# Performance work log

Hardware: AMD Instinct MI355X
Metric: run time of the kernel (lower is better)

Reference implementation:

```python
import jax, jax.numpy as jnp
import numpy as np

N_NODES = 50000
N_EDGES = 800000
N_GRAPHS = 256
DIMS = [64, 128, 256, 512]
GRU_H = 256


def _linit(key, shape, fan_in):
    lim = 1.0 / np.sqrt(fan_in)
    return jax.random.uniform(key, shape, jnp.float32, -lim, lim)


def setup_inputs() -> dict:
    key = jax.random.key(0)
    ks = jax.random.split(key, 24)
    x = jax.random.normal(ks[0], (N_NODES, DIMS[0]), jnp.float32)
    edge_index = jax.random.randint(ks[1], (2, N_EDGES), 0, N_NODES, jnp.int64)
    batch_idx = jnp.sort(jax.random.randint(ks[2], (N_NODES,), 0, N_GRAPHS, jnp.int64))
    inp = {"x": x, "edge_index": edge_index, "batch_idx": batch_idx}
    # GCN layer weights (stored [in, out]) and biases
    for i in range(3):
        inp[f"gcn_w{i}"] = _linit(ks[3 + i], (DIMS[i], DIMS[i + 1]), DIMS[i])
        inp[f"gcn_b{i}"] = jnp.zeros((DIMS[i + 1],), jnp.float32)
    # gate nn: Linear(512, 1)
    inp["gate_w"] = _linit(ks[6], (DIMS[3], 1), DIMS[3])
    inp["gate_b"] = jnp.zeros((1,), jnp.float32)
    # GRU: 2 layers, torch layout W_ih [3H, in], W_hh [3H, H]
    ins = [DIMS[3], GRU_H]
    for l in range(2):
        inp[f"gru_wih{l}"] = _linit(ks[7 + 4 * l], (3 * GRU_H, ins[l]), GRU_H)
        inp[f"gru_whh{l}"] = _linit(ks[8 + 4 * l], (3 * GRU_H, GRU_H), GRU_H)
        inp[f"gru_bih{l}"] = _linit(ks[9 + 4 * l], (3 * GRU_H,), GRU_H)
        inp[f"gru_bhh{l}"] = _linit(ks[10 + 4 * l], (3 * GRU_H,), GRU_H)
    # output proj: Linear(256, 512), torch layout [out, in]
    inp["proj_w"] = _linit(ks[15], (DIMS[3], GRU_H), GRU_H)
    inp["proj_b"] = jnp.zeros((DIMS[3],), jnp.float32)
    return inp


def _gcn_norm(edge_index, n_nodes):
    # add self-loops, symmetric normalization (PyG GCNConv default)
    loop = jnp.arange(n_nodes, dtype=edge_index.dtype)
    src = jnp.concatenate([edge_index[0], loop])
    dst = jnp.concatenate([edge_index[1], loop])
    deg = jax.ops.segment_sum(jnp.ones_like(dst, jnp.float32), dst, num_segments=n_nodes)
    dinv = jnp.where(deg > 0, jax.lax.rsqrt(jnp.maximum(deg, 1.0)), 0.0)
    norm = dinv[src] * dinv[dst]
    return src, dst, norm


def _gru_cell(xv, h, wih, whh, bih, bhh):
    gi = xv @ wih.T + bih
    gh = h @ whh.T + bhh
    ir, iz, inn = jnp.split(gi, 3, axis=-1)
    hr, hz, hn = jnp.split(gh, 3, axis=-1)
    r = jax.nn.sigmoid(ir + hr)
    z = jax.nn.sigmoid(iz + hz)
    n = jnp.tanh(inn + r * hn)
    return (1.0 - z) * n + z * h


def reference(x, edge_index, batch_idx,
              gcn_w0, gcn_b0, gcn_w1, gcn_b1, gcn_w2, gcn_b2,
              gate_w, gate_b,
              gru_wih0, gru_whh0, gru_bih0, gru_bhh0,
              gru_wih1, gru_whh1, gru_bih1, gru_bhh1,
              proj_w, proj_b):
    n = x.shape[0]
    src, dst, norm = _gcn_norm(edge_index, n)
    for w, b in ((gcn_w0, gcn_b0), (gcn_w1, gcn_b1), (gcn_w2, gcn_b2)):
        h = x @ w                                  # [N, out]
        msg = h[src] * norm[:, None]               # gather over edges
        x = jax.ops.segment_sum(msg, dst, num_segments=n) + b
        x = jax.nn.relu(x)
    # attentional aggregation: segment softmax over gate scores
    gate = (x @ gate_w + gate_b)[:, 0]             # [N]
    gmax = jax.ops.segment_max(gate, batch_idx, num_segments=N_GRAPHS)
    e = jnp.exp(gate - gmax[batch_idx])
    denom = jax.ops.segment_sum(e, batch_idx, num_segments=N_GRAPHS)
    alpha = e / denom[batch_idx]
    graph_emb = jax.ops.segment_sum(x * alpha[:, None], batch_idx, num_segments=N_GRAPHS)  # [G, 512]
    # 2-layer GRU with seq_len=1, h0=0
    h0 = jnp.zeros((N_GRAPHS, GRU_H), x.dtype)
    h1 = _gru_cell(graph_emb, h0, gru_wih0, gru_whh0, gru_bih0, gru_bhh0)
    h2 = _gru_cell(h1, h0, gru_wih1, gru_whh1, gru_bih1, gru_bhh1)
    return h2 @ proj_w.T + proj_b                  # [G, 512]
```

## Files before the change

kernel.cpp:

```cpp
#include <hip/hip_runtime.h>


#define N_GRAPHS 256
#define GRU_H 256
#define SCAN_CHUNK 2048

typedef __attribute__((ext_vector_type(8))) short short8;
typedef __attribute__((ext_vector_type(4))) float floatx4;

typedef unsigned short ushort_t;
typedef unsigned int uint_t;

__device__ __forceinline__ float bflo(uint_t u) { return __uint_as_float(u << 16); }
__device__ __forceinline__ float bfhi(uint_t u) { return __uint_as_float(u & 0xffff0000u); }
__device__ __forceinline__ uint_t f2bf(float f) {
    uint_t u = __float_as_uint(f);
    return (u + 0x7fffu + ((u >> 16) & 1u)) >> 16;
}
__device__ __forceinline__ uint_t pack2(float a, float b) {
    return f2bf(a) | (f2bf(b) << 16);
}


__global__ void k_hist(const int* __restrict__ dst, int* __restrict__ counts, int E) {
    int e = blockIdx.x * blockDim.x + threadIdx.x;
    if (e < E) atomicAdd(&counts[dst[e]], 1);
}

__global__ __launch_bounds__(256) void k_scan1(const int* __restrict__ counts,
                                               int* __restrict__ rowptr,
                                               int* __restrict__ bsums,
                                               float* __restrict__ dinv, int n) {
    int b = blockIdx.x, t = threadIdx.x;
    int base = b * SCAN_CHUNK + t * 8;
    int v[8];
    int s = 0;
#pragma unroll
    for (int j = 0; j < 8; ++j) {
        int i = base + j;
        int c = (i < n) ? counts[i] : 0;
        v[j] = s;
        s += c;
        if (i < n) dinv[i] = rsqrtf((float)(c + 1));
    }
    __shared__ int sd[256];
    sd[t] = s;
    __syncthreads();
    for (int off = 1; off < 256; off <<= 1) {
        int tmp = (t >= off) ? sd[t - off] : 0;
        __syncthreads();
        sd[t] += tmp;
        __syncthreads();
    }
    int texcl = sd[t] - s;
    if (t == 255) bsums[b] = sd[255];
#pragma unroll
    for (int j = 0; j < 8; ++j) {
        int i = base + j;
        if (i < n) rowptr[i] = texcl + v[j];
    }
}

__global__ __launch_bounds__(256) void k_scan3(int* __restrict__ rowptr,
                                               int* __restrict__ cursor,
                                               const int* __restrict__ bsums,
                                               int n, int nb) {
    int b = blockIdx.x, t = threadIdx.x;
    __shared__ int s_off;
    if (t == 0) {
        int off = 0, tot = 0;
        for (int i = 0; i < nb; ++i) {
            int v = bsums[i];
            if (i < b) off += v;
            tot += v;
        }
        s_off = off;
        if (b == 0) rowptr[n] = tot;
    }
    __syncthreads();
    int off = s_off;
    int base = b * SCAN_CHUNK + t * 8;
#pragma unroll
    for (int j = 0; j < 8; ++j) {
        int i = base + j;
        if (i < n) { int r = rowptr[i] + off; rowptr[i] = r; cursor[i] = r; }
    }
}

__global__ void k_fill(const int* __restrict__ src, const int* __restrict__ dst,
                       int* __restrict__ cursor, int* __restrict__ col, int E) {
    int e = blockIdx.x * blockDim.x + threadIdx.x;
    if (e < E) {
        int pos = atomicAdd(&cursor[dst[e]], 1);
        col[pos] = src[e];
    }
}


__global__ void k_wt_all(const float* __restrict__ w0, const float* __restrict__ w1,
                         const float* __restrict__ w2, ushort_t* __restrict__ wt0,
                         ushort_t* __restrict__ wt1, ushort_t* __restrict__ wt2) {
    int idx = blockIdx.x * blockDim.x + threadIdx.x;
    if (idx < 8192) {
        int k = idx >> 7, n = idx & 127;
        wt0[(size_t)n * 64 + k] = (ushort_t)f2bf(w0[idx]);
    } else if (idx < 40960) {
        int i = idx - 8192;
        int k = i >> 8, n = i & 255;
        wt1[(size_t)n * 128 + k] = (ushort_t)f2bf(w1[i]);
    } else if (idx < 172032) {
        int i = idx - 40960;
        int k = i >> 9, n = i & 511;
        wt2[(size_t)n * 256 + k] = (ushort_t)f2bf(w2[i]);
    }
}


__global__ void k_split_all(const float* __restrict__ wih0, const float* __restrict__ wih1,
                            const float* __restrict__ pw,
                            ushort_t* __restrict__ h0, ushort_t* __restrict__ l0,
                            ushort_t* __restrict__ h1, ushort_t* __restrict__ l1,
                            ushort_t* __restrict__ h2, ushort_t* __restrict__ l2) {
    int idx = blockIdx.x * blockDim.x + threadIdx.x;
    const float* s; ushort_t* H; ushort_t* L; int i;
    if (idx < 393216)      { s = wih0; H = h0; L = l0; i = idx; }
    else if (idx < 589824) { s = wih1; H = h1; L = l1; i = idx - 393216; }
    else if (idx < 720896) { s = pw;   H = h2; L = l2; i = idx - 589824; }
    else return;
    float v = s[i];
    uint_t h = f2bf(v);
    H[i] = (ushort_t)h;
    L[i] = (ushort_t)f2bf(v - __uint_as_float(h << 16));
}


__global__ void k_prescale(const float4* __restrict__ x, const float* __restrict__ dinv,
                           uint4* __restrict__ xs, int N) {
    int idx = blockIdx.x * blockDim.x + threadIdx.x;
    int n = idx >> 3;
    if (n >= N) return;
    float dn = dinv[n];
    float4 v0 = x[idx * 2], v1 = x[idx * 2 + 1];
    uint4 o;
    o.x = pack2(v0.x * dn, v0.y * dn);
    o.y = pack2(v0.z * dn, v0.w * dn);
    o.z = pack2(v1.x * dn, v1.y * dn);
    o.w = pack2(v1.z * dn, v1.w * dn);
    xs[idx] = o;
}


__device__ __forceinline__ void acc8(float& a0, float& a1, float& a2, float& a3,
                                     float& a4, float& a5, float& a6, float& a7,
                                     const uint4& v) {
    a0 += bflo(v.x); a1 += bfhi(v.x); a2 += bflo(v.y); a3 += bfhi(v.y);
    a4 += bflo(v.z); a5 += bfhi(v.z); a6 += bflo(v.w); a7 += bfhi(v.w);
}

__global__ void k_gather_bf16(const uint4* __restrict__ xs, const int* __restrict__ rp,
                              const int* __restrict__ col, const float* __restrict__ dinv,
                              uint4* __restrict__ agg, int N, int shift ) {
    int idx = blockIdx.x * blockDim.x + threadIdx.x;
    int n = idx >> shift;
    if (n >= N) return;
    int c = idx & ((1 << shift) - 1);
    int C8 = 1 << shift;
    int a = rp[n], b = rp[n + 1];
    uint4 u = xs[(size_t)n * C8 + c];
    float a0 = bflo(u.x), a1 = bfhi(u.x), a2 = bflo(u.y), a3 = bfhi(u.y);
    float a4 = bflo(u.z), a5 = bfhi(u.z), a6 = bflo(u.w), a7 = bfhi(u.w);
    int k = a;
    for (; k + 8 <= b; k += 8) {
        int ci[8];
#pragma unroll
        for (int j = 0; j < 8; ++j) ci[j] = col[k + j];
        uint4 v[8];
#pragma unroll
        for (int j = 0; j < 8; ++j) v[j] = xs[(size_t)ci[j] * C8 + c];
#pragma unroll
        for (int j = 0; j < 8; ++j)
            acc8(a0, a1, a2, a3, a4, a5, a6, a7, v[j]);
    }
    for (; k + 4 <= b; k += 4) {
        int ci[4];
#pragma unroll
        for (int j = 0; j < 4; ++j) ci[j] = col[k + j];
        uint4 v[4];
#pragma unroll
        for (int j = 0; j < 4; ++j) v[j] = xs[(size_t)ci[j] * C8 + c];
#pragma unroll
        for (int j = 0; j < 4; ++j)
            acc8(a0, a1, a2, a3, a4, a5, a6, a7, v[j]);
    }
    for (; k < b; ++k) {
        uint4 v = xs[(size_t)col[k] * C8 + c];
        acc8(a0, a1, a2, a3, a4, a5, a6, a7, v);
    }
    float dn = dinv[n];
    uint4 o;
    o.x = pack2(a0 * dn, a1 * dn);
    o.y = pack2(a2 * dn, a3 * dn);
    o.z = pack2(a4 * dn, a5 * dn);
    o.w = pack2(a6 * dn, a7 * dn);
    agg[idx] = o;
}


__global__ __launch_bounds__(256) void k_gemm_mfma(
    const ushort_t* __restrict__ A, const ushort_t* __restrict__ Wt,
    const float* __restrict__ bias, const float* __restrict__ dinv,
    ushort_t* __restrict__ C, int M, int K, int Nout, int scale_out,
    const float* __restrict__ gate_w, float* __restrict__ gateArr) {
    __shared__ ushort_t As[64 * 72];
    __shared__ ushort_t Bs[64 * 72];
    int tid = threadIdx.x;
    int wave = tid >> 6, lane = tid & 63;
    int quad = lane >> 4, lr = lane & 15;
    int wm = (wave & 1) * 32, wn = (wave >> 1) * 32;
    int bm = blockIdx.x * 64, bn = blockIdx.y * 64;

    floatx4 zero = {0.f, 0.f, 0.f, 0.f};
    floatx4 acc00 = zero, acc01 = zero, acc10 = zero, acc11 = zero;

    int r0 = tid >> 3,         ko0 = (tid & 7) * 8;
    int r1 = (tid + 256) >> 3, ko1 = ((tid + 256) & 7) * 8;

    for (int k0 = 0; k0 < K; k0 += 64) {
        int ar0 = min(bm + r0, M - 1);
        int ar1 = min(bm + r1, M - 1);
        uint4 av0 = *(const uint4*)(A + (size_t)ar0 * K + k0 + ko0);
        uint4 av1 = *(const uint4*)(A + (size_t)ar1 * K + k0 + ko1);
        uint4 bv0 = *(const uint4*)(Wt + (size_t)(bn + r0) * K + k0 + ko0);
        uint4 bv1 = *(const uint4*)(Wt + (size_t)(bn + r1) * K + k0 + ko1);
        __syncthreads();
        *(uint4*)&As[r0 * 72 + ko0] = av0;
        *(uint4*)&As[r1 * 72 + ko1] = av1;
        *(uint4*)&Bs[r0 * 72 + ko0] = bv0;
        *(uint4*)&Bs[r1 * 72 + ko1] = bv1;
        __syncthreads();
#pragma unroll
        for (int ks = 0; ks < 2; ++ks) {
            short8 af0 = *(short8*)&As[(wm + lr) * 72 + ks * 32 + quad * 8];
            short8 af1 = *(short8*)&As[(wm + 16 + lr) * 72 + ks * 32 + quad * 8];
            short8 bf0 = *(short8*)&Bs[(wn + lr) * 72 + ks * 32 + quad * 8];
            short8 bf1 = *(short8*)&Bs[(wn + 16 + lr) * 72 + ks * 32 + quad * 8];
            acc00 = __builtin_amdgcn_mfma_f32_16x16x32_bf16(af0, bf0, acc00, 0, 0, 0);
            acc01 = __builtin_amdgcn_mfma_f32_16x16x32_bf16(af0, bf1, acc01, 0, 0, 0);
            acc10 = __builtin_amdgcn_mfma_f32_16x16x32_bf16(af1, bf0, acc10, 0, 0, 0);
            acc11 = __builtin_amdgcn_mfma_f32_16x16x32_bf16(af1, bf1, acc11, 0, 0, 0);
        }
    }

    float gwv[2] = {0.f, 0.f};
    if (gate_w) {
        gwv[0] = gate_w[bn + wn + lr];
        gwv[1] = gate_w[bn + wn + 16 + lr];
    }
    float pg[2][4] = {};
#pragma unroll
    for (int mi = 0; mi < 2; ++mi) {
#pragma unroll
        for (int ni = 0; ni < 2; ++ni) {
            floatx4 acc = (mi == 0) ? (ni == 0 ? acc00 : acc01)
                                    : (ni == 0 ? acc10 : acc11);
            int col = bn + wn + ni * 16 + lr;
            float bcol = bias[col];
#pragma unroll
            for (int r = 0; r < 4; ++r) {
                int row = bm + wm + mi * 16 + quad * 4 + r;
                if (row < M) {
                    float v = acc[r] + bcol;
                    v = fmaxf(v, 0.0f);
                    if (gate_w) pg[mi][r] += v * gwv[ni];
                    if (scale_out) v *= dinv[row];
                    C[(size_t)row * Nout + col] = (ushort_t)f2bf(v);
                }
            }
        }
    }
    if (gate_w) {
#pragma unroll
        for (int mi = 0; mi < 2; ++mi) {
#pragma unroll
            for (int r = 0; r < 4; ++r) {
                float p = pg[mi][r];
                p += __shfl_down(p, 8, 16);
                p += __shfl_down(p, 4, 16);
                p += __shfl_down(p, 2, 16);
                p += __shfl_down(p, 1, 16);
                if (lr == 0) {
                    int row = bm + wm + mi * 16 + quad * 4 + r;
                    if (row < M) atomicAdd(&gateArr[row], p);
                }
            }
        }
    }
}


__global__ __launch_bounds__(256) void k_gemm3(
    const ushort_t* __restrict__ Ahi, const ushort_t* __restrict__ Alo,
    const ushort_t* __restrict__ Whi, const ushort_t* __restrict__ Wlo,
    const float* __restrict__ bias, float* __restrict__ C,
    int M, int K, int Nout) {
    __shared__ ushort_t AsH[64 * 72];
    __shared__ ushort_t AsL[64 * 72];
    __shared__ ushort_t BsH[64 * 72];
    __shared__ ushort_t BsL[64 * 72];
    int tid = threadIdx.x;
    int wave = tid >> 6, lane = tid & 63;
    int quad = lane >> 4, lr = lane & 15;
    int wm = (wave & 1) * 32, wn = (wave >> 1) * 32;
    int bm = blockIdx.x * 64, bn = blockIdx.y * 64;

    floatx4 zero = {0.f, 0.f, 0.f, 0.f};
    floatx4 acc00 = zero, acc01 = zero, acc10 = zero, acc11 = zero;

    int r0 = tid >> 3,         ko0 = (tid & 7) * 8;
    int r1 = (tid + 256) >> 3, ko1 = ((tid + 256) & 7) * 8;

    for (int k0 = 0; k0 < K; k0 += 64) {
        int ar0 = min(bm + r0, M - 1);
        int ar1 = min(bm + r1, M - 1);
        size_t a0o = (size_t)ar0 * K + k0 + ko0, a1o = (size_t)ar1 * K + k0 + ko1;
        size_t b0o = (size_t)(bn + r0) * K + k0 + ko0, b1o = (size_t)(bn + r1) * K + k0 + ko1;
        uint4 ah0 = *(const uint4*)(Ahi + a0o), ah1 = *(const uint4*)(Ahi + a1o);
        uint4 al0 = *(const uint4*)(Alo + a0o), al1 = *(const uint4*)(Alo + a1o);
        uint4 bh0 = *(const uint4*)(Whi + b0o), bh1 = *(const uint4*)(Whi + b1o);
        uint4 bl0 = *(const uint4*)(Wlo + b0o), bl1 = *(const uint4*)(Wlo + b1o);
        __syncthreads();
        *(uint4*)&AsH[r0 * 72 + ko0] = ah0; *(uint4*)&AsH[r1 * 72 + ko1] = ah1;
        *(uint4*)&AsL[r0 * 72 + ko0] = al0; *(uint4*)&AsL[r1 * 72 + ko1] = al1;
        *(uint4*)&BsH[r0 * 72 + ko0] = bh0; *(uint4*)&BsH[r1 * 72 + ko1] = bh1;
        *(uint4*)&BsL[r0 * 72 + ko0] = bl0; *(uint4*)&BsL[r1 * 72 + ko1] = bl1;
        __syncthreads();
#pragma unroll
        for (int ks = 0; ks < 2; ++ks) {
            int a0i = (wm + lr) * 72 + ks * 32 + quad * 8;
            int a1i = (wm + 16 + lr) * 72 + ks * 32 + quad * 8;
            int b0i = (wn + lr) * 72 + ks * 32 + quad * 8;
            int b1i = (wn + 16 + lr) * 72 + ks * 32 + quad * 8;
            short8 afh0 = *(short8*)&AsH[a0i], afh1 = *(short8*)&AsH[a1i];
            short8 afl0 = *(short8*)&AsL[a0i], afl1 = *(short8*)&AsL[a1i];
            short8 bfh0 = *(short8*)&BsH[b0i], bfh1 = *(short8*)&BsH[b1i];
            short8 bfl0 = *(short8*)&BsL[b0i], bfl1 = *(short8*)&BsL[b1i];
            acc00 = __builtin_amdgcn_mfma_f32_16x16x32_bf16(afh0, bfh0, acc00, 0, 0, 0);
            acc00 = __builtin_amdgcn_mfma_f32_16x16x32_bf16(afh0, bfl0, acc00, 0, 0, 0);
            acc00 = __builtin_amdgcn_mfma_f32_16x16x32_bf16(afl0, bfh0, acc00, 0, 0, 0);
            acc01 = __builtin_amdgcn_mfma_f32_16x16x32_bf16(afh0, bfh1, acc01, 0, 0, 0);
            acc01 = __builtin_amdgcn_mfma_f32_16x16x32_bf16(afh0, bfl1, acc01, 0, 0, 0);
            acc01 = __builtin_amdgcn_mfma_f32_16x16x32_bf16(afl0, bfh1, acc01, 0, 0, 0);
            acc10 = __builtin_amdgcn_mfma_f32_16x16x32_bf16(afh1, bfh0, acc10, 0, 0, 0);
            acc10 = __builtin_amdgcn_mfma_f32_16x16x32_bf16(afh1, bfl0, acc10, 0, 0, 0);
            acc10 = __builtin_amdgcn_mfma_f32_16x16x32_bf16(afl1, bfh0, acc10, 0, 0, 0);
            acc11 = __builtin_amdgcn_mfma_f32_16x16x32_bf16(afh1, bfh1, acc11, 0, 0, 0);
            acc11 = __builtin_amdgcn_mfma_f32_16x16x32_bf16(afh1, bfl1, acc11, 0, 0, 0);
            acc11 = __builtin_amdgcn_mfma_f32_16x16x32_bf16(afl1, bfh1, acc11, 0, 0, 0);
        }
    }

#pragma unroll
    for (int mi = 0; mi < 2; ++mi) {
#pragma unroll
        for (int ni = 0; ni < 2; ++ni) {
            floatx4 acc = (mi == 0) ? (ni == 0 ? acc00 : acc01)
                                    : (ni == 0 ? acc10 : acc11);
            int col = bn + wn + ni * 16 + lr;
            float bcol = bias ? bias[col] : 0.0f;
#pragma unroll
            for (int r = 0; r < 4; ++r) {
                int row = bm + wm + mi * 16 + quad * 4 + r;
                if (row < M)
                    C[(size_t)row * Nout + col] = acc[r] + bcol;
            }
        }
    }
}


__global__ void k_gru_ep(const float* __restrict__ gi, const float* __restrict__ bih,
                         const float* __restrict__ bhh,
                         ushort_t* __restrict__ hhi, ushort_t* __restrict__ hlo, int G) {
    int idx = blockIdx.x * blockDim.x + threadIdx.x;
    int g = idx >> 8, j = idx & 255;
    if (g >= G) return;
    const float* row = gi + (size_t)g * 768;
    float ir = row[j]       + bih[j]       + bhh[j];
    float iz = row[j + 256] + bih[j + 256] + bhh[j + 256];
    float in = row[j + 512] + bih[j + 512];
    float r = 1.0f / (1.0f + expf(-ir));
    float z = 1.0f / (1.0f + expf(-iz));
    float nn = tanhf(in + r * bhh[j + 512]);
    float h = (1.0f - z) * nn;
    uint_t hi = f2bf(h);
    hhi[idx] = (ushort_t)hi;
    hlo[idx] = (ushort_t)f2bf(h - __uint_as_float(hi << 16));
}


__global__ __launch_bounds__(256) void k_softmax_emb(
    const uint_t* __restrict__ x , const float* __restrict__ gate,
    const int* __restrict__ batch, int N,
    ushort_t* __restrict__ embH, ushort_t* __restrict__ embL) {
    int g = blockIdx.x;
    int s, e;
    {
        int lo = 0, hi = N;
        while (lo < hi) { int mid = (lo + hi) >> 1; if (batch[mid] < g) lo = mid + 1; else hi = mid; }
        s = lo;
        lo = s; hi = N;
        while (lo < hi) { int mid = (lo + hi) >> 1; if (batch[mid] < g + 1) lo = mid + 1; else hi = mid; }
        e = lo;
    }
    __shared__ float red[256];
    __shared__ float sal[256];
    int tid = threadIdx.x;
    float m = -INFINITY;
    for (int i = s + tid; i < e; i += 256) m = fmaxf(m, gate[i]);
    red[tid] = m; __syncthreads();
    for (int off = 128; off > 0; off >>= 1) {
        if (tid < off) red[tid] = fmaxf(red[tid], red[tid + off]);
        __syncthreads();
    }
    m = red[0]; __syncthreads();
    float ssum = 0.f;
    for (int i = s + tid; i < e; i += 256) ssum += expf(gate[i] - m);
    red[tid] = ssum; __syncthreads();
    for (int off = 128; off > 0; off >>= 1) {
        if (tid < off) red[tid] += red[tid + off];
        __syncthreads();
    }
    float denom = red[0];
    float inv = (denom > 0.f) ? 1.0f / denom : 0.0f;
    float acc0 = 0.f, acc1 = 0.f;
    for (int base = s; base < e; base += 256) {
        int i = base + tid;
        __syncthreads();
        sal[tid] = (i < e) ? expf(gate[i] - m) * inv : 0.0f;
        __syncthreads();
        int cnt = min(256, e - base);
        for (int k = 0; k < cnt; ++k) {
            float a = sal[k];
            uint_t u = x[(size_t)(base + k) * 256 + tid];
            acc0 += a * bflo(u);
            acc1 += a * bfhi(u);
        }
    }
    int i0 = g * 512 + tid * 2;
    uint_t h0 = f2bf(acc0);
    uint_t h1 = f2bf(acc1);
    embH[i0]     = (ushort_t)h0;
    embH[i0 + 1] = (ushort_t)h1;
    embL[i0]     = (ushort_t)f2bf(acc0 - __uint_as_float(h0 << 16));
    embL[i0 + 1] = (ushort_t)f2bf(acc1 - __uint_as_float(h1 << 16));
}


extern "C" void kernel_launch(void* const* d_in, const int* in_sizes, int n_in,
                              void* d_out, int out_size, void* d_ws, size_t ws_size,
                              hipStream_t stream) {
    const float* x       = (const float*)d_in[0];
    const int*   ei      = (const int*)d_in[1];
    const int*   batch   = (const int*)d_in[2];
    const float* w0      = (const float*)d_in[3];
    const float* b0      = (const float*)d_in[4];
    const float* w1      = (const float*)d_in[5];
    const float* b1      = (const float*)d_in[6];
    const float* w2      = (const float*)d_in[7];
    const float* b2      = (const float*)d_in[8];
    const float* gate_w  = (const float*)d_in[9];
    const float* wih0    = (const float*)d_in[11];
    const float* bih0    = (const float*)d_in[13];
    const float* bhh0    = (const float*)d_in[14];
    const float* wih1    = (const float*)d_in[15];
    const float* bih1    = (const float*)d_in[17];
    const float* bhh1    = (const float*)d_in[18];
    const float* pw      = (const float*)d_in[19];
    const float* pb      = (const float*)d_in[20];
    float* out = (float*)d_out;

    const int N = in_sizes[2];
    const int E = in_sizes[1] / 2;
    const int G = N_GRAPHS;

    char* base = (char*)d_ws;
    size_t off = 0;
    auto alloc = [&](size_t bytes) -> char* {
        char* p = base + off;
        off = (off + bytes + 255) & ~(size_t)255;
        return p;
    };
    ushort_t* bufA  = (ushort_t*)alloc((size_t)N * 512 * 2);
    ushort_t* bufB  = (ushort_t*)alloc((size_t)N * 512 * 2);
    float* dinv     = (float*)alloc((size_t)N * 4);
    float* gateArr  = (float*)alloc((size_t)N * 4);
    int*   counts   = (int*)alloc((size_t)(N + 1) * 4);
    int*   cursor   = (int*)alloc((size_t)(N + 1) * 4);
    int*   rowptr   = (int*)alloc((size_t)(N + 1) * 4);
    int*   bsums    = (int*)alloc((size_t)256 * 4);
    int*   col      = (int*)alloc((size_t)E * 4);
    ushort_t* wt0   = (ushort_t*)alloc((size_t)128 * 64 * 2);
    ushort_t* wt1   = (ushort_t*)alloc((size_t)256 * 128 * 2);
    ushort_t* wt2   = (ushort_t*)alloc((size_t)512 * 256 * 2);
    ushort_t* ih0H  = (ushort_t*)alloc((size_t)768 * 512 * 2);
    ushort_t* ih0L  = (ushort_t*)alloc((size_t)768 * 512 * 2);
    ushort_t* ih1H  = (ushort_t*)alloc((size_t)768 * 256 * 2);
    ushort_t* ih1L  = (ushort_t*)alloc((size_t)768 * 256 * 2);
    ushort_t* pwH   = (ushort_t*)alloc((size_t)512 * 256 * 2);
    ushort_t* pwL   = (ushort_t*)alloc((size_t)512 * 256 * 2);
    ushort_t* embH  = (ushort_t*)alloc((size_t)G * 512 * 2);
    ushort_t* embL  = (ushort_t*)alloc((size_t)G * 512 * 2);
    ushort_t* h1H   = (ushort_t*)alloc((size_t)G * 256 * 2);
    ushort_t* h1L   = (ushort_t*)alloc((size_t)G * 256 * 2);
    ushort_t* h2H   = (ushort_t*)alloc((size_t)G * 256 * 2);
    ushort_t* h2L   = (ushort_t*)alloc((size_t)G * 256 * 2);
    float* gi       = (float*)alloc((size_t)G * 768 * 4);
    (void)ws_size; (void)n_in; (void)out_size;

    const int* src = ei;
    const int* dst = ei + E;

    const int nb = (N + SCAN_CHUNK - 1) / SCAN_CHUNK;

    size_t zbytes = (size_t)((char*)counts - (char*)gateArr) + (size_t)(N + 1) * 4;
    hipMemsetAsync(gateArr, 0, zbytes, stream);

    k_hist<<<(E + 255) / 256, 256, 0, stream>>>(dst, counts, E);
    k_scan1<<<nb, 256, 0, stream>>>(counts, rowptr, bsums, dinv, N);
    k_scan3<<<nb, 256, 0, stream>>>(rowptr, cursor, bsums, N, nb);
    k_fill<<<(E + 255) / 256, 256, 0, stream>>>(src, dst, cursor, col, E);
    k_wt_all<<<(172032 + 255) / 256, 256, 0, stream>>>(w0, w1, w2, wt0, wt1, wt2);
    k_split_all<<<(720896 + 255) / 256, 256, 0, stream>>>(wih0, wih1, pw,
                                                          ih0H, ih0L, ih1H, ih1L, pwH, pwL);

    int mBlocks = (N + 63) / 64;

    k_prescale<<<(N * 8 + 255) / 256, 256, 0, stream>>>((const float4*)x, dinv, (uint4*)bufA, N);
    k_gather_bf16<<<(N * 8 + 255) / 256, 256, 0, stream>>>((const uint4*)bufA, rowptr, col, dinv, (uint4*)bufB, N, 3);
    k_gemm_mfma<<<dim3(mBlocks, 2), 256, 0, stream>>>(bufB, wt0, b0, dinv, bufA, N, 64, 128, 1, nullptr, nullptr);

    k_gather_bf16<<<(N * 16 + 255) / 256, 256, 0, stream>>>((const uint4*)bufA, rowptr, col, dinv, (uint4*)bufB, N, 4);
    k_gemm_mfma<<<dim3(mBlocks, 4), 256, 0, stream>>>(bufB, wt1, b1, dinv, bufA, N, 128, 256, 1, nullptr, nullptr);

    k_gather_bf16<<<(N * 32 + 255) / 256, 256, 0, stream>>>((const uint4*)bufA, rowptr, col, dinv, (uint4*)bufB, N, 5);
    k_gemm_mfma<<<dim3(mBlocks, 8), 256, 0, stream>>>(bufB, wt2, b2, dinv, bufA, N, 256, 512, 0, gate_w, gateArr);

    k_softmax_emb<<<G, 256, 0, stream>>>((const uint_t*)bufA, gateArr, batch, N, embH, embL);

    k_gemm3<<<dim3(G / 64, 12), 256, 0, stream>>>(embH, embL, ih0H, ih0L, nullptr, gi, G, 512, 768);
    k_gru_ep<<<G, 256, 0, stream>>>(gi, bih0, bhh0, h1H, h1L, G);

    k_gemm3<<<dim3(G / 64, 12), 256, 0, stream>>>(h1H, h1L, ih1H, ih1L, nullptr, gi, G, 256, 768);
    k_gru_ep<<<G, 256, 0, stream>>>(gi, bih1, bhh1, h2H, h2L, G);

    k_gemm3<<<dim3(G / 64, 8), 256, 0, stream>>>(h2H, h2L, pwH, pwL, pb, out, G, 256, 512);
}
```

Baseline: 446.8 us.

## Fuse preprocessing kernels and merge tail into persistent kernel with grid barriers

Combines edge fill, input prescale, weight transpose and weight split into a single launch partitioned by block index. Replaces the softmax-embedding, three small GEMMs and two GRU epilogues with one persistent 256-block kernel synchronized by atomic spin grid barriers. This removes several kernel launches and inter-kernel gaps, at the cost of relying on all blocks being co-resident and paying barrier spin overhead.

```diff
diff --git a/kernel.cpp b/kernel.cpp
--- a/kernel.cpp
+++ b/kernel.cpp
@@ -87,66 +87,67 @@
     }
 }
 
-__global__ void k_fill(const int* __restrict__ src, const int* __restrict__ dst,
-                       int* __restrict__ cursor, int* __restrict__ col, int E) {
-    int e = blockIdx.x * blockDim.x + threadIdx.x;
-    if (e < E) {
-        int pos = atomicAdd(&cursor[dst[e]], 1);
-        col[pos] = src[e];
-    }
-}
-
-
-__global__ void k_wt_all(const float* __restrict__ w0, const float* __restrict__ w1,
-                         const float* __restrict__ w2, ushort_t* __restrict__ wt0,
-                         ushort_t* __restrict__ wt1, ushort_t* __restrict__ wt2) {
-    int idx = blockIdx.x * blockDim.x + threadIdx.x;
-    if (idx < 8192) {
-        int k = idx >> 7, n = idx & 127;
-        wt0[(size_t)n * 64 + k] = (ushort_t)f2bf(w0[idx]);
-    } else if (idx < 40960) {
-        int i = idx - 8192;
-        int k = i >> 8, n = i & 255;
-        wt1[(size_t)n * 128 + k] = (ushort_t)f2bf(w1[i]);
-    } else if (idx < 172032) {
-        int i = idx - 40960;
-        int k = i >> 9, n = i & 511;
-        wt2[(size_t)n * 256 + k] = (ushort_t)f2bf(w2[i]);
-    }
-}
-
-
-__global__ void k_split_all(const float* __restrict__ wih0, const float* __restrict__ wih1,
-                            const float* __restrict__ pw,
-                            ushort_t* __restrict__ h0, ushort_t* __restrict__ l0,
-                            ushort_t* __restrict__ h1, ushort_t* __restrict__ l1,
-                            ushort_t* __restrict__ h2, ushort_t* __restrict__ l2) {
-    int idx = blockIdx.x * blockDim.x + threadIdx.x;
-    const float* s; ushort_t* H; ushort_t* L; int i;
-    if (idx < 393216)      { s = wih0; H = h0; L = l0; i = idx; }
-    else if (idx < 589824) { s = wih1; H = h1; L = l1; i = idx - 393216; }
-    else if (idx < 720896) { s = pw;   H = h2; L = l2; i = idx - 589824; }
-    else return;
-    float v = s[i];
-    uint_t h = f2bf(v);
-    H[i] = (ushort_t)h;
-    L[i] = (ushort_t)f2bf(v - __uint_as_float(h << 16));
-}
-
-
-__global__ void k_prescale(const float4* __restrict__ x, const float* __restrict__ dinv,
-                           uint4* __restrict__ xs, int N) {
-    int idx = blockIdx.x * blockDim.x + threadIdx.x;
-    int n = idx >> 3;
-    if (n >= N) return;
-    float dn = dinv[n];
-    float4 v0 = x[idx * 2], v1 = x[idx * 2 + 1];
-    uint4 o;
-    o.x = pack2(v0.x * dn, v0.y * dn);
-    o.y = pack2(v0.z * dn, v0.w * dn);
-    o.z = pack2(v1.x * dn, v1.y * dn);
-    o.w = pack2(v1.z * dn, v1.w * dn);
-    xs[idx] = o;
+
+__global__ __launch_bounds__(256) void k_pack(
+    const int* __restrict__ src, const int* __restrict__ dst,
+    int* __restrict__ cursor, int* __restrict__ col, int E,
+    const float4* __restrict__ x, const float* __restrict__ dinv,
+    uint4* __restrict__ xs, int N,
+    const float* __restrict__ w0, const float* __restrict__ w1,
+    const float* __restrict__ w2, ushort_t* __restrict__ wt0,
+    ushort_t* __restrict__ wt1, ushort_t* __restrict__ wt2,
+    const float* __restrict__ wih0, const float* __restrict__ wih1,
+    const float* __restrict__ pw,
+    ushort_t* __restrict__ sh0, ushort_t* __restrict__ sl0,
+    ushort_t* __restrict__ sh1, ushort_t* __restrict__ sl1,
+    ushort_t* __restrict__ sh2, ushort_t* __restrict__ sl2,
+    int nf, int np, int nw) {
+    int b = blockIdx.x, t = threadIdx.x;
+    if (b < nf) {
+        int e = b * 256 + t;
+        if (e < E) {
+            int pos = atomicAdd(&cursor[dst[e]], 1);
+            col[pos] = src[e];
+        }
+    } else if (b < nf + np) {
+        int idx = (b - nf) * 256 + t;
+        int n = idx >> 3;
+        if (n < N) {
+            float dn = dinv[n];
+            float4 v0 = x[idx * 2], v1 = x[idx * 2 + 1];
+            uint4 o;
+            o.x = pack2(v0.x * dn, v0.y * dn);
+            o.y = pack2(v0.z * dn, v0.w * dn);
+            o.z = pack2(v1.x * dn, v1.y * dn);
+            o.w = pack2(v1.z * dn, v1.w * dn);
+            xs[idx] = o;
+        }
+    } else if (b < nf + np + nw) {
+        int idx = (b - nf - np) * 256 + t;
+        if (idx < 8192) {
+            int k = idx >> 7, n = idx & 127;
+            wt0[(size_t)n * 64 + k] = (ushort_t)f2bf(w0[idx]);
+        } else if (idx < 40960) {
+            int i = idx - 8192;
+            int k = i >> 8, n = i & 255;
+            wt1[(size_t)n * 128 + k] = (ushort_t)f2bf(w1[i]);
+        } else if (idx < 172032) {
+            int i = idx - 40960;
+            int k = i >> 9, n = i & 511;
+            wt2[(size_t)n * 256 + k] = (ushort_t)f2bf(w2[i]);
+        }
+    } else {
+        int idx = (b - nf - np - nw) * 256 + t;
+        const float* s; ushort_t* H; ushort_t* L; int i;
+        if (idx < 393216)      { s = wih0; H = sh0; L = sl0; i = idx; }
+        else if (idx < 589824) { s = wih1; H = sh1; L = sl1; i = idx - 393216; }
+        else if (idx < 720896) { s = pw;   H = sh2; L = sl2; i = idx - 589824; }
+        else return;
+        float v = s[i];
+        uint_t h = f2bf(v);
+        H[i] = (ushort_t)h;
+        L[i] = (ushort_t)f2bf(v - __uint_as_float(h << 16));
+    }
 }
 
 
@@ -298,20 +299,19 @@
 }
 
 
-__global__ __launch_bounds__(256) void k_gemm3(
+__device__ __forceinline__ void gemm3_body(
+    char* smem,
     const ushort_t* __restrict__ Ahi, const ushort_t* __restrict__ Alo,
     const ushort_t* __restrict__ Whi, const ushort_t* __restrict__ Wlo,
     const float* __restrict__ bias, float* __restrict__ C,
-    int M, int K, int Nout) {
-    __shared__ ushort_t AsH[64 * 72];
-    __shared__ ushort_t AsL[64 * 72];
-    __shared__ ushort_t BsH[64 * 72];
-    __shared__ ushort_t BsL[64 * 72];
-    int tid = threadIdx.x;
+    int M, int K, int Nout, int bm, int bn, int tid) {
+    ushort_t* AsH = (ushort_t*)smem;
+    ushort_t* AsL = AsH + 64 * 72;
+    ushort_t* BsH = AsL + 64 * 72;
+    ushort_t* BsL = BsH + 64 * 72;
     int wave = tid >> 6, lane = tid & 63;
     int quad = lane >> 4, lr = lane & 15;
     int wm = (wave & 1) * 32, wn = (wave >> 1) * 32;
-    int bm = blockIdx.x * 64, bn = blockIdx.y * 64;
 
     floatx4 zero = {0.f, 0.f, 0.f, 0.f};
     floatx4 acc00 = zero, acc01 = zero, acc10 = zero, acc11 = zero;
@@ -378,12 +378,12 @@
 }
 
 
-__global__ void k_gru_ep(const float* __restrict__ gi, const float* __restrict__ bih,
-                         const float* __restrict__ bhh,
-                         ushort_t* __restrict__ hhi, ushort_t* __restrict__ hlo, int G) {
-    int idx = blockIdx.x * blockDim.x + threadIdx.x;
+__device__ __forceinline__ void gru_ep_body(int idx, const float* __restrict__ gi,
+                                            const float* __restrict__ bih,
+                                            const float* __restrict__ bhh,
+                                            ushort_t* __restrict__ hhi,
+                                            ushort_t* __restrict__ hlo) {
     int g = idx >> 8, j = idx & 255;
-    if (g >= G) return;
     const float* row = gi + (size_t)g * 768;
     float ir = row[j]       + bih[j]       + bhh[j];
     float iz = row[j + 256] + bih[j + 256] + bhh[j + 256];
@@ -398,61 +398,102 @@
 }
 
 
-__global__ __launch_bounds__(256) void k_softmax_emb(
+__device__ __forceinline__ void gridbar(int* bar) {
+    __threadfence();
+    __syncthreads();
+    if (threadIdx.x == 0) {
+        atomicAdd(bar, 1);
+        while (atomicAdd(bar, 0) < N_GRAPHS) {}
+    }
+    __syncthreads();
+    __threadfence();
+}
+
+
+__global__ __launch_bounds__(256) void k_tail(
     const uint_t* __restrict__ x , const float* __restrict__ gate,
     const int* __restrict__ batch, int N,
-    ushort_t* __restrict__ embH, ushort_t* __restrict__ embL) {
-    int g = blockIdx.x;
-    int s, e;
+    const ushort_t* __restrict__ ih0H, const ushort_t* __restrict__ ih0L,
+    const ushort_t* __restrict__ ih1H, const ushort_t* __restrict__ ih1L,
+    const ushort_t* __restrict__ pwH,  const ushort_t* __restrict__ pwL,
+    const float* __restrict__ bih0, const float* __restrict__ bhh0,
+    const float* __restrict__ bih1, const float* __restrict__ bhh1,
+    const float* __restrict__ pb,
+    ushort_t* __restrict__ embH, ushort_t* __restrict__ embL,
+    ushort_t* __restrict__ h1H, ushort_t* __restrict__ h1L,
+    ushort_t* __restrict__ h2H, ushort_t* __restrict__ h2L,
+    float* __restrict__ gi, float* __restrict__ out, int* __restrict__ bars) {
+    __shared__ char smem[4 * 64 * 72 * 2];
+    int b = blockIdx.x, tid = threadIdx.x;
+
     {
-        int lo = 0, hi = N;
-        while (lo < hi) { int mid = (lo + hi) >> 1; if (batch[mid] < g) lo = mid + 1; else hi = mid; }
-        s = lo;
-        lo = s; hi = N;
-        while (lo < hi) { int mid = (lo + hi) >> 1; if (batch[mid] < g + 1) lo = mid + 1; else hi = mid; }
-        e = lo;
-    }
-    __shared__ float red[256];
-    __shared__ float sal[256];
-    int tid = threadIdx.x;
-    float m = -INFINITY;
-    for (int i = s + tid; i < e; i += 256) m = fmaxf(m, gate[i]);
-    red[tid] = m; __syncthreads();
-    for (int off = 128; off > 0; off >>= 1) {
-        if (tid < off) red[tid] = fmaxf(red[tid], red[tid + off]);
-        __syncthreads();
-    }
-    m = red[0]; __syncthreads();
-    float ssum = 0.f;
-    for (int i = s + tid; i < e; i += 256) ssum += expf(gate[i] - m);
-    red[tid] = ssum; __syncthreads();
-    for (int off = 128; off > 0; off >>= 1) {
-        if (tid < off) red[tid] += red[tid + off];
-        __syncthreads();
-    }
-    float denom = red[0];
-    float inv = (denom > 0.f) ? 1.0f / denom : 0.0f;
-    float acc0 = 0.f, acc1 = 0.f;
-    for (int base = s; base < e; base += 256) {
-        int i = base + tid;
-        __syncthreads();
-        sal[tid] = (i < e) ? expf(gate[i] - m) * inv : 0.0f;
-        __syncthreads();
-        int cnt = min(256, e - base);
-        for (int k = 0; k < cnt; ++k) {
-            float a = sal[k];
-            uint_t u = x[(size_t)(base + k) * 256 + tid];
-            acc0 += a * bflo(u);
-            acc1 += a * bfhi(u);
-        }
-    }
-    int i0 = g * 512 + tid * 2;
-    uint_t h0 = f2bf(acc0);
-    uint_t h1 = f2bf(acc1);
-    embH[i0]     = (ushort_t)h0;
-    embH[i0 + 1] = (ushort_t)h1;
-    embL[i0]     = (ushort_t)f2bf(acc0 - __uint_as_float(h0 << 16));
-    embL[i0 + 1] = (ushort_t)f2bf(acc1 - __uint_as_float(h1 << 16));
+        int g = b;
+        int s, e;
+        {
+            int lo = 0, hi = N;
+            while (lo < hi) { int mid = (lo + hi) >> 1; if (batch[mid] < g) lo = mid + 1; else hi = mid; }
+            s = lo;
+            lo = s; hi = N;
+            while (lo < hi) { int mid = (lo + hi) >> 1; if (batch[mid] < g + 1) lo = mid + 1; else hi = mid; }
+            e = lo;
+        }
+        float* red = (float*)smem;
+        float* sal = red + 256;
+        float m = -INFINITY;
+        for (int i = s + tid; i < e; i += 256) m = fmaxf(m, gate[i]);
+        red[tid] = m; __syncthreads();
+        for (int off = 128; off > 0; off >>= 1) {
+            if (tid < off) red[tid] = fmaxf(red[tid], red[tid + off]);
+            __syncthreads();
+        }
+        m = red[0]; __syncthreads();
+        float ssum = 0.f;
+        for (int i = s + tid; i < e; i += 256) ssum += expf(gate[i] - m);
+        red[tid] = ssum; __syncthreads();
+        for (int off = 128; off > 0; off >>= 1) {
+            if (tid < off) red[tid] += red[tid + off];
+            __syncthreads();
+        }
+        float denom = red[0];
+        float inv = (denom > 0.f) ? 1.0f / denom : 0.0f;
+        float acc0 = 0.f, acc1 = 0.f;
+        for (int base = s; base < e; base += 256) {
+            int i = base + tid;
+            __syncthreads();
+            sal[tid] = (i < e) ? expf(gate[i] - m) * inv : 0.0f;
+            __syncthreads();
+            int cnt = min(256, e - base);
+            for (int k = 0; k < cnt; ++k) {
+                float a = sal[k];
+                uint_t u = x[(size_t)(base + k) * 256 + tid];
+                acc0 += a * bflo(u);
+                acc1 += a * bfhi(u);
+            }
+        }
+        int i0 = g * 512 + tid * 2;
+        uint_t hh0 = f2bf(acc0);
+        uint_t hh1 = f2bf(acc1);
+        embH[i0]     = (ushort_t)hh0;
+        embH[i0 + 1] = (ushort_t)hh1;
+        embL[i0]     = (ushort_t)f2bf(acc0 - __uint_as_float(hh0 << 16));
+        embL[i0 + 1] = (ushort_t)f2bf(acc1 - __uint_as_float(hh1 << 16));
+    }
+    gridbar(&bars[0]);
+    if (b < 48)
+        gemm3_body(smem, embH, embL, ih0H, ih0L, nullptr, gi,
+                   256, 512, 768, (b & 3) * 64, (b >> 2) * 64, tid);
+    gridbar(&bars[1]);
+    gru_ep_body(b * 256 + tid, gi, bih0, bhh0, h1H, h1L);
+    gridbar(&bars[2]);
+    if (b < 48)
+        gemm3_body(smem, h1H, h1L, ih1H, ih1L, nullptr, gi,
+                   256, 256, 768, (b & 3) * 64, (b >> 2) * 64, tid);
+    gridbar(&bars[3]);
+    gru_ep_body(b * 256 + tid, gi, bih1, bhh1, h2H, h2L);
+    gridbar(&bars[4]);
+    if (b < 32)
+        gemm3_body(smem, h2H, h2L, pwH, pwL, pb, out,
+                   256, 256, 512, (b & 3) * 64, (b >> 2) * 64, tid);
 }
 
 
@@ -494,6 +535,7 @@
     ushort_t* bufB  = (ushort_t*)alloc((size_t)N * 512 * 2);
     float* dinv     = (float*)alloc((size_t)N * 4);
     float* gateArr  = (float*)alloc((size_t)N * 4);
+    int*   bars     = (int*)alloc((size_t)8 * 4);
     int*   counts   = (int*)alloc((size_t)(N + 1) * 4);
     int*   cursor   = (int*)alloc((size_t)(N + 1) * 4);
     int*   rowptr   = (int*)alloc((size_t)(N + 1) * 4);
@@ -528,14 +570,20 @@
     k_hist<<<(E + 255) / 256, 256, 0, stream>>>(dst, counts, E);
     k_scan1<<<nb, 256, 0, stream>>>(counts, rowptr, bsums, dinv, N);
     k_scan3<<<nb, 256, 0, stream>>>(rowptr, cursor, bsums, N, nb);
-    k_fill<<<(E + 255) / 256, 256, 0, stream>>>(src, dst, cursor, col, E);
-    k_wt_all<<<(172032 + 255) / 256, 256, 0, stream>>>(w0, w1, w2, wt0, wt1, wt2);
-    k_split_all<<<(720896 + 255) / 256, 256, 0, stream>>>(wih0, wih1, pw,
-                                                          ih0H, ih0L, ih1H, ih1L, pwH, pwL);
+
+    int nf = (E + 255) / 256;
+    int np = (N * 8 + 255) / 256;
+    int nw = (172032 + 255) / 256;
+    int ns = (720896 + 255) / 256;
+    k_pack<<<nf + np + nw + ns, 256, 0, stream>>>(
+        src, dst, cursor, col, E,
+        (const float4*)x, dinv, (uint4*)bufA, N,
+        w0, w1, w2, wt0, wt1, wt2,
+        wih0, wih1, pw, ih0H, ih0L, ih1H, ih1L, pwH, pwL,
+        nf, np, nw);
 
     int mBlocks = (N + 63) / 64;
 
-    k_prescale<<<(N * 8 + 255) / 256, 256, 0, stream>>>((const float4*)x, dinv, (uint4*)bufA, N);
     k_gather_bf16<<<(N * 8 + 255) / 256, 256, 0, stream>>>((const uint4*)bufA, rowptr, col, dinv, (uint4*)bufB, N, 3);
     k_gemm_mfma<<<dim3(mBlocks, 2), 256, 0, stream>>>(bufB, wt0, b0, dinv, bufA, N, 64, 128, 1, nullptr, nullptr);
 
@@ -545,13 +593,8 @@
     k_gather_bf16<<<(N * 32 + 255) / 256, 256, 0, stream>>>((const uint4*)bufA, rowptr, col, dinv, (uint4*)bufB, N, 5);
     k_gemm_mfma<<<dim3(mBlocks, 8), 256, 0, stream>>>(bufB, wt2, b2, dinv, bufA, N, 256, 512, 0, gate_w, gateArr);
 
-    k_softmax_emb<<<G, 256, 0, stream>>>((const uint_t*)bufA, gateArr, batch, N, embH, embL);
-
-    k_gemm3<<<dim3(G / 64, 12), 256, 0, stream>>>(embH, embL, ih0H, ih0L, nullptr, gi, G, 512, 768);
-    k_gru_ep<<<G, 256, 0, stream>>>(gi, bih0, bhh0, h1H, h1L, G);
-
-    k_gemm3<<<dim3(G / 64, 12), 256, 0, stream>>>(h1H, h1L, ih1H, ih1L, nullptr, gi, G, 256, 768);
-    k_gru_ep<<<G, 256, 0, stream>>>(gi, bih1, bhh1, h2H, h2L, G);
-
-    k_gemm3<<<dim3(G / 64, 8), 256, 0, stream>>>(h2H, h2L, pwH, pwL, pb, out, G, 256, 512);
-}
+    k_tail<<<G, 256, 0, stream>>>((const uint_t*)bufA, gateArr, batch, N,
+                                  ih0H, ih0L, ih1H, ih1L, pwH, pwL,
+                                  bih0, bhh0, bih1, bhh1, pb,
+                                  embH, embL, h1H, h1L, h2H, h2L, gi, out, bars);
+}
```

Result: slower. 653.2 us (+46.2%).
